# Optimization experiments

Hardware: AMD Instinct MI355X
Metric: run time of the kernel (lower is better)

The kernel has to match this reference:

```python
import jax, jax.numpy as jnp
import numpy as np

N = 50000       # num nodes
E = 800000      # num edges (avg degree 16)
D_IN = 128
D_H = 128
D_LAT = 64
BN_EPS = 1e-5


def _glorot(key, fan_in, fan_out):
    return jax.random.normal(key, (fan_in, fan_out), jnp.float32) / np.sqrt(fan_in).astype(np.float32)


def setup_inputs() -> dict:
    key = jax.random.key(0)
    ks = jax.random.split(key, 8)
    x = jax.random.normal(ks[0], (N, D_IN), jnp.float32)
    edge_index = jax.random.randint(ks[1], (2, E), 0, N)  # row 0 = src, row 1 = dst
    return {
        "x": x,
        "edge_index": edge_index,
        "W0": _glorot(ks[2], D_IN, D_H),
        "W1": _glorot(ks[3], D_H, D_H),
        "W_mu": _glorot(ks[4], D_H, D_LAT),
        "W_logvar": _glorot(ks[5], D_H, D_LAT),
        "gamma0": jnp.ones((D_H,), jnp.float32),
        "beta0": jnp.zeros((D_H,), jnp.float32),
        "gamma1": jnp.ones((D_H,), jnp.float32),
        "beta1": jnp.zeros((D_H,), jnp.float32),
    }


def _gcn_conv(h, W, src, dst, dinv):
    # Standard GCN with self-loops: D^{-1/2}(A+I)D^{-1/2} (X W)
    m = h @ W                                   # [N, out]
    coef = (dinv[src] * dinv[dst])[:, None]     # [E, 1]
    out = jax.ops.segment_sum(m[src] * coef, dst, num_segments=N)
    return out + m * (dinv * dinv)[:, None]     # self-loop contribution


def _batchnorm(h, gamma, beta):
    mean = jnp.mean(h, axis=0)
    var = jnp.var(h, axis=0)
    return (h - mean) * jax.lax.rsqrt(var + BN_EPS) * gamma + beta


def reference(x, edge_index, W0, W1, W_mu, W_logvar, gamma0, beta0, gamma1, beta1):
    # decoder_type='graph', augment_type=None, used_edge_weight=False,
    # use_FCencoder=False, num_domains=1; dropout is identity in reference.
    src, dst = edge_index[0], edge_index[1]
    deg = jax.ops.segment_sum(jnp.ones((E,), x.dtype), dst, num_segments=N) + 1.0
    dinv = jax.lax.rsqrt(deg)

    h = _gcn_conv(x, W0, src, dst, dinv)
    h = jax.nn.relu(_batchnorm(h, gamma0, beta0))
    h = _gcn_conv(h, W1, src, dst, dinv)
    h = jax.nn.relu(_batchnorm(h, gamma1, beta1))

    z_mean = _gcn_conv(h, W_mu, src, dst, dinv)
    z_log_std = _gcn_conv(h, W_logvar, src, dst, dinv)
    return (z_mean, z_log_std)
```

## Files before the change

kernel.cpp:

```cpp
#include <hip/hip_runtime.h>
#include <hip/hip_bf16.h>


static __device__ __forceinline__ unsigned short f2bf(float f) {
    __hip_bfloat16 h = __float2bfloat16(f);
    return *reinterpret_cast<unsigned short*>(&h);
}
static __device__ __forceinline__ float bf_lo(unsigned int u) {
    return __uint_as_float(u << 16);
}
static __device__ __forceinline__ float bf_hi(unsigned int u) {
    return __uint_as_float(u & 0xffff0000u);
}

__global__ __launch_bounds__(256)
void deg_count(const int* __restrict__ ei, int* __restrict__ cnt, int E_) {
    int e = blockIdx.x * 256 + threadIdx.x;
    if (e < E_) atomicAdd(&cnt[ei[E_ + e]], 1);
}

__global__ __launch_bounds__(1024)
void scan_blocks(const int* __restrict__ cnt, float* __restrict__ dinv,
                 int* __restrict__ rowptr, int* __restrict__ partials, int n) {
    __shared__ int ls[1024];
    int tid = threadIdx.x;
    int i = blockIdx.x * 1024 + tid;
    int v = (i < n) ? cnt[i] : 0;
    if (i < n) dinv[i] = rsqrtf((float)v + 1.0f);
    ls[tid] = v;
    __syncthreads();
    #pragma unroll
    for (int off = 1; off < 1024; off <<= 1) {
        int t = (tid >= off) ? ls[tid - off] : 0;
        __syncthreads();
        ls[tid] += t;
        __syncthreads();
    }
    if (i < n) rowptr[i] = ls[tid] - v;
    if (tid == 1023) partials[blockIdx.x] = ls[1023];
}

__global__ __launch_bounds__(1024)
void scan_partials(int* __restrict__ partials, int* __restrict__ rowptr_n,
                   int nb) {
    __shared__ int ls[1024];
    int tid = threadIdx.x;
    int v = (tid < nb) ? partials[tid] : 0;
    ls[tid] = v;
    __syncthreads();
    #pragma unroll
    for (int off = 1; off < 1024; off <<= 1) {
        int t = (tid >= off) ? ls[tid - off] : 0;
        __syncthreads();
        ls[tid] += t;
        __syncthreads();
    }
    if (tid < nb) partials[tid] = ls[tid] - v;
    if (tid == 1023) *rowptr_n = ls[1023];
}

__global__ __launch_bounds__(256)
void scan_add(int* __restrict__ rowptr, int* __restrict__ cursor,
              const int* __restrict__ partials, int n) {
    int i = blockIdx.x * 256 + threadIdx.x;
    if (i < n) {
        int v = rowptr[i] + partials[i >> 10];
        rowptr[i] = v;
        cursor[i] = v;
    }
}

__global__ __launch_bounds__(256)
void csr_fill(const int* __restrict__ ei, const float* __restrict__ dinv,
              int* __restrict__ cursor, unsigned int* __restrict__ csr, int E_) {
    int e = blockIdx.x * 256 + threadIdx.x;
    if (e >= E_) return;
    int s = ei[e], d = ei[E_ + e];
    float coef = dinv[s] * dinv[d];
    unsigned int cb = (__float_as_uint(coef) + 0x8000u) >> 16;
    int p = atomicAdd(&cursor[d], 1);
    csr[p] = ((unsigned int)s << 15) | (cb & 0x7fffu);
}

__global__ __launch_bounds__(128)
void bn_coef(const float* __restrict__ stats, const float* __restrict__ gamma,
             const float* __restrict__ beta, float* __restrict__ sc,
             float* __restrict__ sh, int n) {
    int c = threadIdx.x;
    float inv_n = 1.0f / (float)n;
    float mean = stats[c] * inv_n;
    float var  = stats[128 + c] * inv_n - mean * mean;
    float s = rsqrtf(var + 1e-5f) * gamma[c];
    sc[c] = s;
    sh[c] = beta[c] - mean * s;
}

template<bool FUSE_BN, bool SPLIT_W, bool XBF>
__global__ __launch_bounds__(256)
void gemm128(const void* __restrict__ Xv, const float* __restrict__ Wa,
             const float* __restrict__ Wb, const float* __restrict__ sc,
             const float* __restrict__ sh, unsigned short* __restrict__ Y,
             int nRows) {
    __shared__ float xs[32][128];
    const int tid = threadIdx.x;
    const int row0 = blockIdx.x * 32;

    if (!XBF) {
        const float* X = (const float*)Xv;
        #pragma unroll
        for (int q = 0; q < 4; ++q) {
            int flat = (q * 256 + tid) * 4;
            int r = flat >> 7, k = flat & 127;
            float4 v = make_float4(0.f, 0.f, 0.f, 0.f);
            if (row0 + r < nRows)
                v = *(const float4*)(X + (size_t)(row0 + r) * 128 + k);
            if (FUSE_BN) {
                float4 s4 = *(const float4*)(sc + k);
                float4 h4 = *(const float4*)(sh + k);
                v.x = fmaxf(v.x * s4.x + h4.x, 0.f);
                v.y = fmaxf(v.y * s4.y + h4.y, 0.f);
                v.z = fmaxf(v.z * s4.z + h4.z, 0.f);
                v.w = fmaxf(v.w * s4.w + h4.w, 0.f);
            }
            *(float4*)&xs[r][k] = v;
        }
    } else {
        const unsigned short* X = (const unsigned short*)Xv;
        #pragma unroll
        for (int q = 0; q < 2; ++q) {
            int flat = (q * 256 + tid) * 8;
            int r = flat >> 7, k = flat & 127;
            uint4 u = make_uint4(0u, 0u, 0u, 0u);
            if (row0 + r < nRows)
                u = *(const uint4*)(X + (size_t)(row0 + r) * 128 + k);
            float v[8] = {bf_lo(u.x), bf_hi(u.x), bf_lo(u.y), bf_hi(u.y),
                          bf_lo(u.z), bf_hi(u.z), bf_lo(u.w), bf_hi(u.w)};
            if (FUSE_BN) {
                float4 sA = *(const float4*)(sc + k);
                float4 sB = *(const float4*)(sc + k + 4);
                float4 hA = *(const float4*)(sh + k);
                float4 hB = *(const float4*)(sh + k + 4);
                v[0] = fmaxf(v[0] * sA.x + hA.x, 0.f);
                v[1] = fmaxf(v[1] * sA.y + hA.y, 0.f);
                v[2] = fmaxf(v[2] * sA.z + hA.z, 0.f);
                v[3] = fmaxf(v[3] * sA.w + hA.w, 0.f);
                v[4] = fmaxf(v[4] * sB.x + hB.x, 0.f);
                v[5] = fmaxf(v[5] * sB.y + hB.y, 0.f);
                v[6] = fmaxf(v[6] * sB.z + hB.z, 0.f);
                v[7] = fmaxf(v[7] * sB.w + hB.w, 0.f);
            }
            #pragma unroll
            for (int j = 0; j < 8; ++j) xs[r][k + j] = v[j];
        }
    }
    __syncthreads();

    const int tx = tid & 31, ty = tid >> 5;
    const int c0 = tx * 4, r0 = ty * 4;
    float acc[4][4] = {};

    for (int k = 0; k < 128; k += 4) {
        float xv[4][4];
        #pragma unroll
        for (int i = 0; i < 4; ++i)
            *(float4*)xv[i] = *(const float4*)&xs[r0 + i][k];
        #pragma unroll
        for (int j = 0; j < 4; ++j) {
            int kk = k + j;
            float4 wv;
            if (!SPLIT_W) {
                wv = *(const float4*)(Wa + kk * 128 + c0);
            } else {
                wv = (c0 < 64) ? *(const float4*)(Wa + kk * 64 + c0)
                               : *(const float4*)(Wb + kk * 64 + (c0 - 64));
            }
            #pragma unroll
            for (int i = 0; i < 4; ++i) {
                acc[i][0] += xv[i][j] * wv.x;
                acc[i][1] += xv[i][j] * wv.y;
                acc[i][2] += xv[i][j] * wv.z;
                acc[i][3] += xv[i][j] * wv.w;
            }
        }
    }

    #pragma unroll
    for (int i = 0; i < 4; ++i) {
        int r = row0 + r0 + i;
        if (r >= nRows) continue;
        ushort4 o;
        o.x = f2bf(acc[i][0]); o.y = f2bf(acc[i][1]);
        o.z = f2bf(acc[i][2]); o.w = f2bf(acc[i][3]);
        *(ushort4*)(Y + (size_t)r * 128 + c0) = o;
    }
}

template<bool TO_OUT>
__global__ __launch_bounds__(256)
void gather_bf(const unsigned short* __restrict__ M,
               const int* __restrict__ rowptr,
               const unsigned int* __restrict__ csr,
               const float* __restrict__ dinv, void* __restrict__ O, int n) {
    int wid  = (blockIdx.x * 256 + threadIdx.x) >> 6;
    int lane = threadIdx.x & 63;
    if (wid >= n) return;
    const unsigned int* m2 = (const unsigned int*)M;

    float di = dinv[wid];
    unsigned int su = m2[(size_t)wid * 64 + lane];
    float c = di * di;
    float a0x = bf_lo(su) * c, a0y = bf_hi(su) * c;
    float a1x = 0.f, a1y = 0.f, a2x = 0.f, a2y = 0.f, a3x = 0.f, a3y = 0.f;

    int beg = __builtin_amdgcn_readfirstlane(rowptr[wid]);
    int end = __builtin_amdgcn_readfirstlane(rowptr[wid + 1]);

    int k = beg;
    for (; k + 3 < end; k += 4) {
        unsigned int e0 = csr[k],     e1 = csr[k + 1];
        unsigned int e2 = csr[k + 2], e3 = csr[k + 3];
        unsigned int u0 = m2[(size_t)(e0 >> 15) * 64 + lane];
        unsigned int u1 = m2[(size_t)(e1 >> 15) * 64 + lane];
        unsigned int u2 = m2[(size_t)(e2 >> 15) * 64 + lane];
        unsigned int u3 = m2[(size_t)(e3 >> 15) * 64 + lane];
        float w0 = __uint_as_float((e0 & 0x7fffu) << 16);
        float w1 = __uint_as_float((e1 & 0x7fffu) << 16);
        float w2 = __uint_as_float((e2 & 0x7fffu) << 16);
        float w3 = __uint_as_float((e3 & 0x7fffu) << 16);
        a0x += w0 * bf_lo(u0); a0y += w0 * bf_hi(u0);
        a1x += w1 * bf_lo(u1); a1y += w1 * bf_hi(u1);
        a2x += w2 * bf_lo(u2); a2y += w2 * bf_hi(u2);
        a3x += w3 * bf_lo(u3); a3y += w3 * bf_hi(u3);
    }
    for (; k < end; ++k) {
        unsigned int e0 = csr[k];
        unsigned int u0 = m2[(size_t)(e0 >> 15) * 64 + lane];
        float w0 = __uint_as_float((e0 & 0x7fffu) << 16);
        a0x += w0 * bf_lo(u0); a0y += w0 * bf_hi(u0);
    }
    float ax = (a0x + a1x) + (a2x + a3x);
    float ay = (a0y + a1y) + (a2y + a3y);

    if (!TO_OUT) {
        unsigned int o = (unsigned int)f2bf(ax) | ((unsigned int)f2bf(ay) << 16);
        ((unsigned int*)O)[(size_t)wid * 64 + lane] = o;
    } else {
        float* Of = (float*)O;
        float* dst = (lane < 32)
            ? Of + (size_t)wid * 64 + 2 * lane
            : Of + (size_t)n * 64 + (size_t)wid * 64 + 2 * (lane - 32);
        *(float2*)dst = make_float2(ax, ay);
    }
}

__global__ __launch_bounds__(256)
void bn_stats(const unsigned short* __restrict__ H, float* __restrict__ stats,
              int n) {
    const uint4* h4 = (const uint4*)H;
    const int tid = threadIdx.x;
    const int cg = tid & 15;
    const int rg = tid >> 4;
    float s[8] = {}, q[8] = {};
    for (int r = blockIdx.x * 16 + rg; r < n; r += gridDim.x * 16) {
        uint4 u = h4[(size_t)r * 16 + cg];
        float v[8] = {bf_lo(u.x), bf_hi(u.x), bf_lo(u.y), bf_hi(u.y),
                      bf_lo(u.z), bf_hi(u.z), bf_lo(u.w), bf_hi(u.w)};
        #pragma unroll
        for (int j = 0; j < 8; ++j) { s[j] += v[j]; q[j] += v[j] * v[j]; }
    }
    __shared__ float ls[256][17];
    #pragma unroll
    for (int j = 0; j < 8; ++j) { ls[tid][j] = s[j]; ls[tid][8 + j] = q[j]; }
    __syncthreads();
    if (tid < 128) {
        int c = tid, cgrp = c >> 3, j = c & 7;
        float S = 0.f, Q = 0.f;
        #pragma unroll
        for (int g = 0; g < 16; ++g) {
            S += ls[(g << 4) | cgrp][j];
            Q += ls[(g << 4) | cgrp][8 + j];
        }
        atomicAdd(&stats[c], S);
        atomicAdd(&stats[128 + c], Q);
    }
}

extern "C" void kernel_launch(void* const* d_in, const int* in_sizes, int n_in,
                              void* d_out, int out_size, void* d_ws, size_t ws_size,
                              hipStream_t stream) {
    const float* x    = (const float*)d_in[0];
    const int*   ei   = (const int*)d_in[1];
    const float* W0   = (const float*)d_in[2];
    const float* W1   = (const float*)d_in[3];
    const float* Wmu  = (const float*)d_in[4];
    const float* Wlog = (const float*)d_in[5];
    const float* g0   = (const float*)d_in[6];
    const float* b0   = (const float*)d_in[7];
    const float* g1   = (const float*)d_in[8];
    const float* b1   = (const float*)d_in[9];

    const int N_ = in_sizes[0] / 128;
    const int E_ = in_sizes[1] / 2;
    float* out = (float*)d_out;

    char* w = (char*)d_ws;
    auto carve = [&](size_t bytes) {
        char* p = w;
        w += (bytes + 255) & ~(size_t)255;
        return p;
    };
    int*   cnt    = (int*)  carve((size_t)N_ * 4);
    float* stats0 = (float*)carve(256 * 4);
    float* stats1 = (float*)carve(256 * 4);
    char*  zend   = w;
    float* dinv   = (float*)carve((size_t)N_ * 4);
    int*   rowptr = (int*)  carve((size_t)(N_ + 1) * 4);
    int*   cursor = (int*)  carve((size_t)(N_ + 1) * 4);
    int*   partials = (int*)carve(1024 * 4);
    unsigned int* csr = (unsigned int*)carve((size_t)E_ * 4);
    float* sc0    = (float*)carve(128 * 4);
    float* sh0    = (float*)carve(128 * 4);
    float* sc1    = (float*)carve(128 * 4);
    float* sh1    = (float*)carve(128 * 4);
    unsigned short* Mbf = (unsigned short*)carve((size_t)N_ * 128 * 2);
    unsigned short* Hb  = (unsigned short*)carve((size_t)N_ * 128 * 2);

    const int gGemm = (N_ + 31) / 32;
    const int gGath = (N_ * 64 + 255) / 256;
    const int nb    = (N_ + 1023) / 1024;

    hipMemsetAsync(cnt, 0, (size_t)(zend - (char*)cnt), stream);
    deg_count<<<(E_ + 255) / 256, 256, 0, stream>>>(ei, cnt, E_);
    scan_blocks<<<nb, 1024, 0, stream>>>(cnt, dinv, rowptr, partials, N_);
    scan_partials<<<1, 1024, 0, stream>>>(partials, rowptr + N_, nb);
    scan_add<<<(N_ + 255) / 256, 256, 0, stream>>>(rowptr, cursor, partials, N_);
    csr_fill<<<(E_ + 255) / 256, 256, 0, stream>>>(ei, dinv, cursor, csr, E_);

    gemm128<false, false, false><<<gGemm, 256, 0, stream>>>(
        x, W0, nullptr, nullptr, nullptr, Mbf, N_);
    gather_bf<false><<<gGath, 256, 0, stream>>>(Mbf, rowptr, csr, dinv, Hb, N_);
    bn_stats<<<512, 256, 0, stream>>>(Hb, stats0, N_);
    bn_coef<<<1, 128, 0, stream>>>(stats0, g0, b0, sc0, sh0, N_);

    gemm128<true, false, true><<<gGemm, 256, 0, stream>>>(
        Hb, W1, nullptr, sc0, sh0, Mbf, N_);
    gather_bf<false><<<gGath, 256, 0, stream>>>(Mbf, rowptr, csr, dinv, Hb, N_);
    bn_stats<<<512, 256, 0, stream>>>(Hb, stats1, N_);
    bn_coef<<<1, 128, 0, stream>>>(stats1, g1, b1, sc1, sh1, N_);

    gemm128<true, true, true><<<gGemm, 256, 0, stream>>>(
        Hb, Wmu, Wlog, sc1, sh1, Mbf, N_);
    gather_bf<true><<<gGath, 256, 0, stream>>>(Mbf, rowptr, csr, dinv, out, N_);
}
```

Before: 320.9 us.

## Replace scalar FP32 GEMM with bf16 MFMA GEMM using swizzled LDS weights

Rewrites the dense node-feature GEMM to use 16x16x32 bf16 MFMA instructions. The weight matrix is converted to bf16, transposed into LDS with an XOR swizzle, and activations are loaded directly into registers. BN+ReLU is fused on the A operand, and each block now handles 128 rows. This removes the FP32 FMA-bound inner loop, at the cost of rounding the first-layer input to bf16 and writing the output with scalar 2-byte stores.

```diff
diff --git a/kernel.cpp b/kernel.cpp
--- a/kernel.cpp
+++ b/kernel.cpp
@@ -1,6 +1,9 @@
 #include <hip/hip_runtime.h>
 #include <hip/hip_bf16.h>
 
+
+using short8 = __attribute__((ext_vector_type(8))) short;
+using f32x4  = __attribute__((ext_vector_type(4))) float;
 
 static __device__ __forceinline__ unsigned short f2bf(float f) {
     __hip_bfloat16 h = __float2bfloat16(f);
@@ -11,6 +14,9 @@
 }
 static __device__ __forceinline__ float bf_hi(unsigned int u) {
     return __uint_as_float(u & 0xffff0000u);
+}
+static __device__ __forceinline__ float bf2f(unsigned short u) {
+    return __uint_as_float((unsigned int)u << 16);
 }
 
 __global__ __launch_bounds__(256)
@@ -95,103 +101,101 @@
     sh[c] = beta[c] - mean * s;
 }
 
-template<bool FUSE_BN, bool SPLIT_W, bool XBF>
-__global__ __launch_bounds__(256)
-void gemm128(const void* __restrict__ Xv, const float* __restrict__ Wa,
-             const float* __restrict__ Wb, const float* __restrict__ sc,
-             const float* __restrict__ sh, unsigned short* __restrict__ Y,
-             int nRows) {
-    __shared__ float xs[32][128];
+template<bool XBF, bool FUSE_BN, bool SPLIT_W>
+__global__ __launch_bounds__(256)
+void gemm_mfma(const void* __restrict__ Xv, const float* __restrict__ Wa,
+               const float* __restrict__ Wb, const float* __restrict__ sc,
+               const float* __restrict__ sh, unsigned short* __restrict__ Y,
+               int nRows) {
+    __shared__ unsigned short wt[128 * 128];
+
     const int tid = threadIdx.x;
-    const int row0 = blockIdx.x * 32;
-
-    if (!XBF) {
-        const float* X = (const float*)Xv;
-        #pragma unroll
-        for (int q = 0; q < 4; ++q) {
-            int flat = (q * 256 + tid) * 4;
-            int r = flat >> 7, k = flat & 127;
-            float4 v = make_float4(0.f, 0.f, 0.f, 0.f);
-            if (row0 + r < nRows)
-                v = *(const float4*)(X + (size_t)(row0 + r) * 128 + k);
-            if (FUSE_BN) {
-                float4 s4 = *(const float4*)(sc + k);
-                float4 h4 = *(const float4*)(sh + k);
-                v.x = fmaxf(v.x * s4.x + h4.x, 0.f);
-                v.y = fmaxf(v.y * s4.y + h4.y, 0.f);
-                v.z = fmaxf(v.z * s4.z + h4.z, 0.f);
-                v.w = fmaxf(v.w * s4.w + h4.w, 0.f);
+
+    #pragma unroll
+    for (int it = 0; it < 16; ++it) {
+        int flat4 = it * 256 + tid;
+        int k  = flat4 >> 5;
+        int c0 = (flat4 & 31) * 4;
+        const float* srcp;
+        if (!SPLIT_W) srcp = Wa + k * 128 + c0;
+        else          srcp = (c0 < 64) ? (Wa + k * 64 + c0)
+                                       : (Wb + k * 64 + (c0 - 64));
+        float4 v = *(const float4*)srcp;
+        float vv[4] = {v.x, v.y, v.z, v.w};
+        #pragma unroll
+        for (int j = 0; j < 4; ++j) {
+            int c = c0 + j;
+            wt[c * 128 + (k ^ ((c & 7) << 3))] = f2bf(vv[j]);
+        }
+    }
+    __syncthreads();
+
+    const int lane = tid & 63;
+    const int wv   = tid >> 6;
+    const int lm   = lane & 15;
+    const int lg   = lane >> 4;
+    const int row0 = blockIdx.x * 128 + wv * 32;
+
+    f32x4 acc[2][8] = {};
+
+    #pragma unroll
+    for (int ks = 0; ks < 4; ++ks) {
+        const int k0 = ks * 32 + lg * 8;
+
+        short8 a[2];
+        #pragma unroll
+        for (int mf = 0; mf < 2; ++mf) {
+            int r = row0 + mf * 16 + lm;
+            if (r < nRows) {
+                if (XBF) {
+                    a[mf] = *(const short8*)((const unsigned short*)Xv +
+                                             (size_t)r * 128 + k0);
+                    if (FUSE_BN) {
+                        float4 s0 = *(const float4*)(sc + k0);
+                        float4 s1 = *(const float4*)(sc + k0 + 4);
+                        float4 h0 = *(const float4*)(sh + k0);
+                        float4 h1 = *(const float4*)(sh + k0 + 4);
+                        float sv[8] = {s0.x, s0.y, s0.z, s0.w, s1.x, s1.y, s1.z, s1.w};
+                        float hv[8] = {h0.x, h0.y, h0.z, h0.w, h1.x, h1.y, h1.z, h1.w};
+                        #pragma unroll
+                        for (int j = 0; j < 8; ++j) {
+                            float v = bf2f((unsigned short)a[mf][j]);
+                            v = fmaxf(v * sv[j] + hv[j], 0.f);
+                            a[mf][j] = (short)f2bf(v);
+                        }
+                    }
+                } else {
+                    const float* xp = (const float*)Xv + (size_t)r * 128 + k0;
+                    float4 p0 = *(const float4*)xp;
+                    float4 p1 = *(const float4*)(xp + 4);
+                    float pv[8] = {p0.x, p0.y, p0.z, p0.w, p1.x, p1.y, p1.z, p1.w};
+                    #pragma unroll
+                    for (int j = 0; j < 8; ++j) a[mf][j] = (short)f2bf(pv[j]);
+                }
+            } else {
+                a[mf] = short8{};
             }
-            *(float4*)&xs[r][k] = v;
-        }
-    } else {
-        const unsigned short* X = (const unsigned short*)Xv;
-        #pragma unroll
-        for (int q = 0; q < 2; ++q) {
-            int flat = (q * 256 + tid) * 8;
-            int r = flat >> 7, k = flat & 127;
-            uint4 u = make_uint4(0u, 0u, 0u, 0u);
-            if (row0 + r < nRows)
-                u = *(const uint4*)(X + (size_t)(row0 + r) * 128 + k);
-            float v[8] = {bf_lo(u.x), bf_hi(u.x), bf_lo(u.y), bf_hi(u.y),
-                          bf_lo(u.z), bf_hi(u.z), bf_lo(u.w), bf_hi(u.w)};
-            if (FUSE_BN) {
-                float4 sA = *(const float4*)(sc + k);
-                float4 sB = *(const float4*)(sc + k + 4);
-                float4 hA = *(const float4*)(sh + k);
-                float4 hB = *(const float4*)(sh + k + 4);
-                v[0] = fmaxf(v[0] * sA.x + hA.x, 0.f);
-                v[1] = fmaxf(v[1] * sA.y + hA.y, 0.f);
-                v[2] = fmaxf(v[2] * sA.z + hA.z, 0.f);
-                v[3] = fmaxf(v[3] * sA.w + hA.w, 0.f);
-                v[4] = fmaxf(v[4] * sB.x + hB.x, 0.f);
-                v[5] = fmaxf(v[5] * sB.y + hB.y, 0.f);
-                v[6] = fmaxf(v[6] * sB.z + hB.z, 0.f);
-                v[7] = fmaxf(v[7] * sB.w + hB.w, 0.f);
-            }
+        }
+
+        #pragma unroll
+        for (int f = 0; f < 8; ++f) {
+            int c = f * 16 + lm;
+            short8 b = *(const short8*)&wt[c * 128 + (k0 ^ ((c & 7) << 3))];
+            acc[0][f] = __builtin_amdgcn_mfma_f32_16x16x32_bf16(a[0], b, acc[0][f], 0, 0, 0);
+            acc[1][f] = __builtin_amdgcn_mfma_f32_16x16x32_bf16(a[1], b, acc[1][f], 0, 0, 0);
+        }
+    }
+
+    #pragma unroll
+    for (int mf = 0; mf < 2; ++mf) {
+        #pragma unroll
+        for (int reg = 0; reg < 4; ++reg) {
+            int r = row0 + mf * 16 + lg * 4 + reg;
+            if (r >= nRows) continue;
             #pragma unroll
-            for (int j = 0; j < 8; ++j) xs[r][k + j] = v[j];
-        }
-    }
-    __syncthreads();
-
-    const int tx = tid & 31, ty = tid >> 5;
-    const int c0 = tx * 4, r0 = ty * 4;
-    float acc[4][4] = {};
-
-    for (int k = 0; k < 128; k += 4) {
-        float xv[4][4];
-        #pragma unroll
-        for (int i = 0; i < 4; ++i)
-            *(float4*)xv[i] = *(const float4*)&xs[r0 + i][k];
-        #pragma unroll
-        for (int j = 0; j < 4; ++j) {
-            int kk = k + j;
-            float4 wv;
-            if (!SPLIT_W) {
-                wv = *(const float4*)(Wa + kk * 128 + c0);
-            } else {
-                wv = (c0 < 64) ? *(const float4*)(Wa + kk * 64 + c0)
-                               : *(const float4*)(Wb + kk * 64 + (c0 - 64));
-            }
-            #pragma unroll
-            for (int i = 0; i < 4; ++i) {
-                acc[i][0] += xv[i][j] * wv.x;
-                acc[i][1] += xv[i][j] * wv.y;
-                acc[i][2] += xv[i][j] * wv.z;
-                acc[i][3] += xv[i][j] * wv.w;
-            }
-        }
-    }
-
-    #pragma unroll
-    for (int i = 0; i < 4; ++i) {
-        int r = row0 + r0 + i;
-        if (r >= nRows) continue;
-        ushort4 o;
-        o.x = f2bf(acc[i][0]); o.y = f2bf(acc[i][1]);
-        o.z = f2bf(acc[i][2]); o.w = f2bf(acc[i][3]);
-        *(ushort4*)(Y + (size_t)r * 128 + c0) = o;
+            for (int f = 0; f < 8; ++f)
+                Y[(size_t)r * 128 + f * 16 + lm] = f2bf(acc[mf][f][reg]);
+        }
     }
 }
 
@@ -325,7 +329,7 @@
     unsigned short* Mbf = (unsigned short*)carve((size_t)N_ * 128 * 2);
     unsigned short* Hb  = (unsigned short*)carve((size_t)N_ * 128 * 2);
 
-    const int gGemm = (N_ + 31) / 32;
+    const int gGemm = (N_ + 127) / 128;
     const int gGath = (N_ * 64 + 255) / 256;
     const int nb    = (N_ + 1023) / 1024;
 
@@ -336,19 +340,19 @@
     scan_add<<<(N_ + 255) / 256, 256, 0, stream>>>(rowptr, cursor, partials, N_);
     csr_fill<<<(E_ + 255) / 256, 256, 0, stream>>>(ei, dinv, cursor, csr, E_);
 
-    gemm128<false, false, false><<<gGemm, 256, 0, stream>>>(
+    gemm_mfma<false, false, false><<<gGemm, 256, 0, stream>>>(
         x, W0, nullptr, nullptr, nullptr, Mbf, N_);
     gather_bf<false><<<gGath, 256, 0, stream>>>(Mbf, rowptr, csr, dinv, Hb, N_);
     bn_stats<<<512, 256, 0, stream>>>(Hb, stats0, N_);
     bn_coef<<<1, 128, 0, stream>>>(stats0, g0, b0, sc0, sh0, N_);
 
-    gemm128<true, false, true><<<gGemm, 256, 0, stream>>>(
+    gemm_mfma<true, true, false><<<gGemm, 256, 0, stream>>>(
         Hb, W1, nullptr, sc0, sh0, Mbf, N_);
     gather_bf<false><<<gGath, 256, 0, stream>>>(Mbf, rowptr, csr, dinv, Hb, N_);
     bn_stats<<<512, 256, 0, stream>>>(Hb, stats1, N_);
     bn_coef<<<1, 128, 0, stream>>>(stats1, g1, b1, sc1, sh1, N_);
 
-    gemm128<true, true, true><<<gGemm, 256, 0, stream>>>(
+    gemm_mfma<true, true, true><<<gGemm, 256, 0, stream>>>(
         Hb, Wmu, Wlog, sc1, sh1, Mbf, N_);
     gather_bf<true><<<gGath, 256, 0, stream>>>(Mbf, rowptr, csr, dinv, out, N_);
 }
```

After: 270.7 us. 15.6% less time.
